# Kernel optimization log

Measured on AMD Instinct MI355X. Metric: run time of the kernel, lower is better.

Reference implementation:

```python
import jax, jax.numpy as jnp
import numpy as np
from jax import lax

B, H, W, C = 4, 32, 32, 256
N_HEADS = 8
HEAD_D = C // N_HEADS  # 32


def position_encoding(height, width, channels):
    # Faithful to Position_Embedding: for size=256, dim=128; both even/odd use sin.
    dim = channels // 2
    y_embed = np.repeat(np.arange(1, height + 1), width).reshape(height, width)
    x_embed = np.broadcast_to(np.arange(1, width + 1), (height, width))
    div_term = 10000.0 ** (2 * (np.arange(dim) // 2) / dim)
    pos_x = x_embed[:, :, None] / div_term
    pos_y = y_embed[:, :, None] / div_term
    px = np.concatenate((np.sin(pos_x[:, :, 0::2]), np.sin(pos_x[:, :, 1::2])), axis=2)
    py = np.concatenate((np.sin(pos_y[:, :, 0::2]), np.sin(pos_y[:, :, 1::2])), axis=2)
    pe = np.concatenate((py, px), axis=2)[None].astype(np.float32)  # [1,H,W,C]
    return jnp.asarray(pe)


def setup_inputs() -> dict:
    key = jax.random.key(0)
    ks = jax.random.split(key, 10)
    s = 0.02  # weight init scale
    return {
        "src1": jax.random.normal(ks[0], (B, H, W, C), jnp.float32),
        "src2": jax.random.normal(ks[1], (B, H, W, C), jnp.float32),
        "Wq1": jax.random.normal(ks[2], (C, C), jnp.float32) * s,
        "bq1": jnp.zeros((C,), jnp.float32),
        "Wq2": jax.random.normal(ks[3], (C, C), jnp.float32) * s,
        "bq2": jnp.zeros((C,), jnp.float32),
        "Wk": jax.random.normal(ks[4], (C, C), jnp.float32) * s,
        "bk": jnp.zeros((C,), jnp.float32),
        "Wv": jax.random.normal(ks[5], (C, C), jnp.float32) * s,
        "bv": jnp.zeros((C,), jnp.float32),
        "conv_w": jax.random.normal(ks[6], (3, 3, 2 * HEAD_D, 2 * HEAD_D), jnp.float32) * s,
        "conv_b": jnp.zeros((2 * HEAD_D,), jnp.float32),
        "Wo": jax.random.normal(ks[7], (C, C), jnp.float32) * s,
        "bo": jnp.zeros((C,), jnp.float32),
    }


def reference(src1, src2, Wq1, bq1, Wq2, bq2, Wk, bk, Wv, bv, conv_w, conv_b, Wo, bo):
    d = HEAD_D
    N = H * W
    pe = position_encoding(H, W, C)  # [1,H,W,C]
    kin = src1 + pe
    q1_in = src1 + pe
    v_in = src1 + pe
    q2_in = src2 + pe

    q1 = q1_in @ Wq1 + bq1  # [B,H,W,C]
    q2 = q2_in @ Wq2 + bq2
    k = kin @ Wk + bk
    v = v_in @ Wv + bv

    # Q head split: 8 heads -> add first 4 and last 4 -> 4 effective heads
    Q1 = q1.reshape(B, N, 8, d)
    q_s_1 = Q1[:, :, :4, :] + Q1[:, :, 4:, :]  # [B,N,4,d]
    Q2 = q2.reshape(B, N, 8, d)
    q_s_2 = Q2[:, :, :4, :] + Q2[:, :, 4:, :]  # [B,N,4,d]

    # K split: self path (first 4d channels), co path (conv on 2d, concat last 2d)
    k_s = k[..., : 4 * d]  # [B,H,W,4d]
    k_co_1 = k[..., 4 * d : 6 * d]  # [B,H,W,2d]
    k_co_2 = k[..., 6 * d :]  # [B,H,W,2d]
    k_conv_r = lax.conv_general_dilated(
        k_co_1, conv_w, window_strides=(1, 1), padding="SAME",
        dimension_numbers=("NHWC", "HWIO", "NHWC")) + conv_b
    k_conv = jnp.concatenate([k_conv_r, k_co_2], axis=-1)  # [B,H,W,4d]

    k_s_1 = k_s.reshape(B, N, 4, d)
    k_s_2 = k_conv.reshape(B, N, 4, d)
    v_co = v.reshape(B, N, 8, d).transpose(0, 2, 1, 3)  # [B,8,N,d]

    scale = jnp.sqrt(jnp.float32(d))
    logits_self = jnp.einsum("bnhd,bmhd->bhnm", q_s_1, k_s_1) / scale  # [B,4,N,N]
    logits_co = jnp.einsum("bnhd,bmhd->bhnm", q_s_2, k_s_2) / scale  # [B,4,N,N]
    scaled = jnp.concatenate([logits_co, logits_self], axis=1)  # [B,8,N,N]

    attn = jax.nn.softmax(scaled, axis=-1)
    out = jnp.einsum("bhnm,bhmd->bnhd", attn, v_co).reshape(B, N, C)
    return out @ Wo + bo  # [B,N,C]
```

## Files before the change

kernel.cpp:

```cpp
#include <hip/hip_runtime.h>
#include <cstdint>
#include <cstddef>

typedef __attribute__((ext_vector_type(8))) short short8v;
typedef __attribute__((ext_vector_type(4))) short short4v;
typedef __attribute__((ext_vector_type(4))) float f32x4;
typedef unsigned short ushort_t;

__device__ inline unsigned short f2bf(float x) {
    unsigned int u = __float_as_uint(x);
    return (unsigned short)((u + 0x7FFFu + ((u >> 16) & 1u)) >> 16);
}

__device__ inline unsigned int cvtpk_bf16(float lo, float hi) {
    unsigned int r;
    asm("v_cvt_pk_bf16_f32 %0, %1, %2" : "=v"(r) : "v"(lo), "v"(hi));
    return r;
}

__global__ __launch_bounds__(256) void pe_prep_kernel(
    const float* __restrict__ src1, const float* __restrict__ src2,
    const float* __restrict__ Wq1, const float* __restrict__ Wq2,
    const float* __restrict__ Wk, const float* __restrict__ Wv,
    const float* __restrict__ Wo, const float* __restrict__ cw,
    const float* __restrict__ bq1, const float* __restrict__ bq2,
    const float* __restrict__ bk, const float* __restrict__ bv,
    ushort_t* __restrict__ X1, ushort_t* __restrict__ X2,
    ushort_t* __restrict__ WcatT, ushort_t* __restrict__ WoT,
    float* __restrict__ bcat, ushort_t* __restrict__ Wcv2)
{
    __shared__ ushort_t Ts[64][72];
    int bx = blockIdx.x;
    int t = threadIdx.x;

    if (bx < 512) {
        int n = bx * 2 + (t >> 7);
        int cp = (t & 127) * 2;
        int row = n >> 5, col = n & 31;
        float pos = (cp < 128) ? (float)(row + 1) : (float)(col + 1);
        float f0 = expf(-0.14391156831212787f * (float)(cp & 63));
        float f1 = expf(-0.14391156831212787f * (float)((cp + 1) & 63));
        float pe0 = sinf(pos * f0);
        float pe1 = sinf(pos * f1);
        #pragma unroll
        for (int b = 0; b < 4; ++b) {
            size_t idx = ((size_t)b * 1024 + n) * 256 + cp;
            float2 s1 = *(const float2*)&src1[idx];
            float2 s2 = *(const float2*)&src2[idx];
            *(unsigned int*)&X1[idx] = cvtpk_bf16(s1.x + pe0, s1.y + pe1);
            *(unsigned int*)&X2[idx] = cvtpk_bf16(s2.x + pe0, s2.y + pe1);
        }
        return;
    }

    if (bx < 576) {
        int idx = bx - 512;
        int kt = idx & 3, ct = idx >> 2;
        int k0 = kt * 64;
        const float* W; int csrc; int fold = 0; ushort_t* dst; int dstbase;
        if (ct < 2)       { W = Wq1; csrc = ct * 64;        fold = 1; dst = WcatT; dstbase = ct * 64; }
        else if (ct < 4)  { W = Wq2; csrc = (ct - 2) * 64;  fold = 1; dst = WcatT; dstbase = ct * 64; }
        else if (ct < 8)  { W = Wk;  csrc = (ct - 4) * 64;            dst = WcatT; dstbase = ct * 64; }
        else if (ct < 12) { W = Wv;  csrc = (ct - 8) * 64;            dst = WcatT; dstbase = ct * 64; }
        else              { W = Wo;  csrc = (ct - 12) * 64;           dst = WoT;   dstbase = (ct - 12) * 64; }
        if (kt == 0) {
            if (ct == 0 && t < 128) bcat[t] = bq1[t] + bq1[t + 128];
            if (ct == 2 && t < 128) bcat[128 + t] = bq2[t] + bq2[t + 128];
            if (ct == 4) bcat[256 + t] = bk[t];
            if (ct == 8) bcat[512 + t] = bv[t];
        }

        int kr = t >> 2, cq = t & 3;
        #pragma unroll
        for (int i = 0; i < 4; ++i) {
            int cc = cq * 16 + i * 4;
            float4 v = *(const float4*)&W[(size_t)(k0 + kr) * 256 + csrc + cc];
            if (fold) {
                float4 v2 = *(const float4*)&W[(size_t)(k0 + kr) * 256 + csrc + cc + 128];
                v.x += v2.x; v.y += v2.y; v.z += v2.z; v.w += v2.w;
            }
            unsigned int u01 = cvtpk_bf16(v.x, v.y);
            unsigned int u23 = cvtpk_bf16(v.z, v.w);
            Ts[kr][cc + 0] = (ushort_t)(u01 & 0xFFFFu); Ts[kr][cc + 1] = (ushort_t)(u01 >> 16);
            Ts[kr][cc + 2] = (ushort_t)(u23 & 0xFFFFu); Ts[kr][cc + 3] = (ushort_t)(u23 >> 16);
        }
        __syncthreads();
        int cr = t >> 2, kq = t & 3;
        ushort_t tmp[16];
        #pragma unroll
        for (int i = 0; i < 16; ++i) tmp[i] = Ts[kq * 16 + i][cr];
        *(short8v*)&dst[(size_t)(dstbase + cr) * 256 + k0 + kq * 16]     = *(short8v*)&tmp[0];
        *(short8v*)&dst[(size_t)(dstbase + cr) * 256 + k0 + kq * 16 + 8] = *(short8v*)&tmp[8];
        return;
    }

    {
        int tap = bx - 576;
        int ci = t >> 2, co0 = (t & 3) * 16;
        #pragma unroll
        for (int i = 0; i < 16; ++i)
            Ts[ci][co0 + i] = f2bf(cw[((size_t)(tap * 64 + ci)) * 64 + co0 + i]);
        __syncthreads();
        int co = t >> 2, ci0 = (t & 3) * 16;
        ushort_t tmp[16];
        #pragma unroll
        for (int i = 0; i < 16; ++i) tmp[i] = Ts[ci0 + i][co];
        int kh = ci0 >> 5;
        int f = (tap * 2 + kh) * 4 + (co >> 4);
        int off = f * 512 + (co & 15) * 32 + (ci0 & 31);
        *(short8v*)&Wcv2[off]     = *(short8v*)&tmp[0];
        *(short8v*)&Wcv2[off + 8] = *(short8v*)&tmp[8];
    }
}

__global__ __launch_bounds__(256) void proj_gemm(
    const ushort_t* __restrict__ X1, const ushort_t* __restrict__ X2,
    const ushort_t* __restrict__ WcatT, const float* __restrict__ bcat,
    ushort_t* __restrict__ Qbf, ushort_t* __restrict__ Kbf,
    ushort_t* __restrict__ VTbf, ushort_t* __restrict__ CVbf)
{
    __shared__ ushort_t As[64][136];
    __shared__ ushort_t Bs[64][136];
    int colBase = blockIdx.x * 64, rowBase = blockIdx.y * 64;
    const ushort_t* A = (colBase >= 128 && colBase < 256) ? X2 : X1;
    int tid = threadIdx.x;
    int w = tid >> 6, l = tid & 63, lr = l & 15, g = l >> 4;
    int wr = w >> 1, wc = w & 1;
    int tr = tid >> 2, tq = tid & 3;
    f32x4 acc[2][2] = {};

    for (int kb = 0; kb < 256; kb += 128) {
        #pragma unroll
        for (int i = 0; i < 4; ++i)
            *(short8v*)&As[tr][tq * 32 + i * 8] =
                *(const short8v*)&A[(size_t)(rowBase + tr) * 256 + kb + tq * 32 + i * 8];
        #pragma unroll
        for (int i = 0; i < 4; ++i)
            *(short8v*)&Bs[tr][tq * 32 + i * 8] =
                *(const short8v*)&WcatT[(size_t)(colBase + tr) * 256 + kb + tq * 32 + i * 8];
        __syncthreads();
        #pragma unroll
        for (int ks = 0; ks < 4; ++ks) {
            short8v a0 = *(const short8v*)&As[wr * 32 + lr][ks * 32 + g * 8];
            short8v a1 = *(const short8v*)&As[wr * 32 + 16 + lr][ks * 32 + g * 8];
            short8v b0 = *(const short8v*)&Bs[wc * 32 + lr][ks * 32 + g * 8];
            short8v b1 = *(const short8v*)&Bs[wc * 32 + 16 + lr][ks * 32 + g * 8];
            acc[0][0] = __builtin_amdgcn_mfma_f32_16x16x32_bf16(a0, b0, acc[0][0], 0, 0, 0);
            acc[0][1] = __builtin_amdgcn_mfma_f32_16x16x32_bf16(a0, b1, acc[0][1], 0, 0, 0);
            acc[1][0] = __builtin_amdgcn_mfma_f32_16x16x32_bf16(a1, b0, acc[1][0], 0, 0, 0);
            acc[1][1] = __builtin_amdgcn_mfma_f32_16x16x32_bf16(a1, b1, acc[1][1], 0, 0, 0);
        }
        __syncthreads();
    }

    const float scale = 0.25503532182457352f;
    #pragma unroll
    for (int fr = 0; fr < 2; ++fr)
        #pragma unroll
        for (int fc = 0; fc < 2; ++fc) {
            int c = colBase + wc * 32 + fc * 16 + lr;
            float bv = bcat[c];
            int nb = rowBase + wr * 32 + fr * 16 + g * 4;
            int b = nb >> 10;
            float vv[4];
            #pragma unroll
            for (int r = 0; r < 4; ++r) vv[r] = acc[fr][fc][r] + bv;
            if (c < 256) {
                #pragma unroll
                for (int r = 0; r < 4; ++r) vv[r] *= scale;
            }
            unsigned int u01 = cvtpk_bf16(vv[0], vv[1]);
            unsigned int u23 = cvtpk_bf16(vv[2], vv[3]);
            ushort_t sv[4] = {(ushort_t)(u01 & 0xFFFFu), (ushort_t)(u01 >> 16),
                              (ushort_t)(u23 & 0xFFFFu), (ushort_t)(u23 >> 16)};
            if (c < 512) {
                #pragma unroll
                for (int r = 0; r < 4; ++r) {
                    int n = nb + r;
                    if (c < 128) {
                        int h = 4 + (c >> 5), d = c & 31;
                        Qbf[(((size_t)(b * 8 + h) << 10) | (n & 1023)) * 32 + d] = sv[r];
                    } else if (c < 256) {
                        int c2 = c - 128;
                        int h = c2 >> 5, d = c2 & 31;
                        Qbf[(((size_t)(b * 8 + h) << 10) | (n & 1023)) * 32 + d] = sv[r];
                    } else {
                        int c3 = c - 256;
                        if (c3 < 128) {
                            int h = 4 + (c3 >> 5), d = c3 & 31;
                            Kbf[(((size_t)(b * 8 + h) << 10) | (n & 1023)) * 32 + d] = sv[r];
                        } else if (c3 < 192) {
                            CVbf[(size_t)n * 64 + (c3 - 128)] = sv[r];
                        } else {
                            int h = 2 + ((c3 - 192) >> 5), d = c3 & 31;
                            Kbf[(((size_t)(b * 8 + h) << 10) | (n & 1023)) * 32 + d] = sv[r];
                        }
                    }
                }
            } else {
                int c4 = c - 512;
                int h = c4 >> 5, d = c4 & 31;
                uint2 pk;
                pk.x = u01; pk.y = u23;
                *(uint2*)&VTbf[((size_t)((b * 8 + h) * 32 + d)) * 1024 + (nb & 1023)] = pk;
            }
        }
}

__global__ __launch_bounds__(256) void conv_mfma(
    const ushort_t* __restrict__ CVbf, const ushort_t* __restrict__ Wcv2,
    const float* __restrict__ cb, ushort_t* __restrict__ Kbf)
{
    __shared__ ushort_t Xs[8704];
    int blk = blockIdx.x;
    int b = blk >> 5, rem = blk & 31;
    int y0 = (rem >> 1) * 2, chalf = rem & 1;
    int tid = threadIdx.x, w = tid >> 6, l = tid & 63, lr = l & 15, g = l >> 4;

    for (int p = tid >> 1; p < 136; p += 128) {
        int ry = p / 34, xc = p % 34;
        int ci0 = (tid & 1) * 32;
        int gy = y0 - 1 + ry, gx = xc - 1;
        int base = p << 6;
        int sw = (xc & 7) << 3;
        if ((unsigned)gy < 32u && (unsigned)gx < 32u) {
            const ushort_t* src = &CVbf[((size_t)(b * 1024 + gy * 32 + gx)) * 64 + ci0];
            #pragma unroll
            for (int k = 0; k < 4; ++k)
                *(short8v*)&Xs[(base + ci0 + k * 8) ^ sw] = *(const short8v*)&src[k * 8];
        } else {
            short8v z = {};
            #pragma unroll
            for (int k = 0; k < 4; ++k)
                *(short8v*)&Xs[(base + ci0 + k * 8) ^ sw] = z;
        }
    }
    __syncthreads();

    int yl = w >> 1, xb = (w & 1) * 16;
    f32x4 acc[2] = {};
    #pragma unroll
    for (int ky = 0; ky < 3; ++ky)
        #pragma unroll
        for (int kx = 0; kx < 3; ++kx) {
            int tap = ky * 3 + kx;
            #pragma unroll
            for (int kh = 0; kh < 2; ++kh) {
                int xa = xb + lr + kx;
                int e = (((yl + ky) * 34 + xa) << 6) + kh * 32 + g * 8;
                short8v af = *(const short8v*)&Xs[e ^ ((xa & 7) << 3)];
                int fb = ((tap * 2 + kh) * 4 + chalf * 2) * 512 + lr * 32 + g * 8;
                #pragma unroll
                for (int nf = 0; nf < 2; ++nf) {
                    short8v bf_ = *(const short8v*)&Wcv2[fb + nf * 512];
                    acc[nf] = __builtin_amdgcn_mfma_f32_16x16x32_bf16(af, bf_, acc[nf], 0, 0, 0);
                }
            }
        }

    #pragma unroll
    for (int nf = 0; nf < 2; ++nf) {
        int co = chalf * 32 + nf * 16 + lr;
        float bias = cb[co];
        int h = chalf, d = nf * 16 + lr;
        unsigned int u01 = cvtpk_bf16(acc[nf][0] + bias, acc[nf][1] + bias);
        unsigned int u23 = cvtpk_bf16(acc[nf][2] + bias, acc[nf][3] + bias);
        ushort_t sv[4] = {(ushort_t)(u01 & 0xFFFFu), (ushort_t)(u01 >> 16),
                          (ushort_t)(u23 & 0xFFFFu), (ushort_t)(u23 >> 16)};
        #pragma unroll
        for (int r = 0; r < 4; ++r) {
            int px = w * 16 + g * 4 + r;
            int n = y0 * 32 + px;
            Kbf[(((size_t)(b * 8 + h) << 10) | n) * 32 + d] = sv[r];
        }
    }
}

__global__ __launch_bounds__(256) void attn_mfma6(
    const ushort_t* __restrict__ Qbf, const ushort_t* __restrict__ Kbf,
    const ushort_t* __restrict__ VTbf, ushort_t* __restrict__ AObf)
{
    __shared__ ushort_t Kt[2][128][32];
    __shared__ ushort_t VT[2][32][136];
    __shared__ ushort_t Ps[4][16][136];

    int bh = blockIdx.y, q0 = blockIdx.x * 64;
    int tid = threadIdx.x, w = tid >> 6, l = tid & 63, lr = l & 15, g = l >> 4;
    int vd = tid >> 3, vn = (tid & 7) * 8;

    short8v qfrag = *(const short8v*)&Qbf[((size_t)bh * 1024 + q0 + w * 16 + lr) * 32 + g * 8];

    f32x4 accO[2] = {};
    float lsum = 0.f;
    const f32x4 zero = {};

    const short8v* Ksrc = (const short8v*)&Kbf[(size_t)bh * 1024 * 32];
    const ushort_t* Vsrc = &VTbf[(size_t)bh * 32 * 1024];

    ((short8v*)&Kt[0][0][0])[tid]       = Ksrc[tid];
    ((short8v*)&Kt[0][0][0])[tid + 256] = Ksrc[tid + 256];
    *(short8v*)&VT[0][vd][vn]      = *(const short8v*)&Vsrc[(size_t)vd * 1024 + vn];
    *(short8v*)&VT[0][vd][vn + 64] = *(const short8v*)&Vsrc[(size_t)vd * 1024 + vn + 64];

    for (int mt = 0; mt < 8; ++mt) {
        int cur = mt & 1, nb = cur ^ 1;
        __syncthreads();

        short8v kreg0, kreg1, vreg0, vreg1;
        bool hasNext = (mt + 1) < 8;
        if (hasNext) {
            int m1 = (mt + 1) * 128;
            kreg0 = Ksrc[m1 * 4 + tid];
            kreg1 = Ksrc[m1 * 4 + tid + 256];
            vreg0 = *(const short8v*)&Vsrc[(size_t)vd * 1024 + m1 + vn];
            vreg1 = *(const short8v*)&Vsrc[(size_t)vd * 1024 + m1 + vn + 64];
        }

        f32x4 st[8];
        #pragma unroll
        for (int t = 0; t < 8; ++t) {
            short8v kf = *(const short8v*)&Kt[cur][t * 16 + lr][g * 8];
            st[t] = __builtin_amdgcn_mfma_f32_16x16x32_bf16(kf, qfrag, zero, 0, 0, 0);
        }

        #pragma unroll
        for (int t = 0; t < 8; ++t) {
            float p0 = exp2f(st[t][0]), p1 = exp2f(st[t][1]);
            float p2 = exp2f(st[t][2]), p3 = exp2f(st[t][3]);
            lsum += (p0 + p1) + (p2 + p3);
            uint2 pw;
            pw.x = cvtpk_bf16(p0, p1);
            pw.y = cvtpk_bf16(p2, p3);
            *(uint2*)&Ps[w][lr][t * 16 + g * 4] = pw;
        }

        #pragma unroll
        for (int kt = 0; kt < 4; ++kt) {
            short8v pa = *(const short8v*)&Ps[w][lr][kt * 32 + g * 8];
            #pragma unroll
            for (int nt = 0; nt < 2; ++nt) {
                short8v vb = *(const short8v*)&VT[cur][nt * 16 + lr][kt * 32 + g * 8];
                accO[nt] = __builtin_amdgcn_mfma_f32_16x16x32_bf16(pa, vb, accO[nt], 0, 0, 0);
            }
        }

        if (hasNext) {
            ((short8v*)&Kt[nb][0][0])[tid]       = kreg0;
            ((short8v*)&Kt[nb][0][0])[tid + 256] = kreg1;
            *(short8v*)&VT[nb][vd][vn]      = vreg0;
            *(short8v*)&VT[nb][vd][vn + 64] = vreg1;
        }
    }

    lsum += __shfl_xor(lsum, 16);
    lsum += __shfl_xor(lsum, 32);

    int b = bh >> 3, h = bh & 7;
    #pragma unroll
    for (int r = 0; r < 4; ++r) {
        float lv = __uint_as_float((unsigned)__builtin_amdgcn_ds_bpermute(
            (g * 4 + r) * 4, (int)__float_as_uint(lsum)));
        float inv = 1.0f / lv;
        int n = q0 + w * 16 + g * 4 + r;
        unsigned int u = cvtpk_bf16(accO[0][r] * inv, accO[1][r] * inv);
        AObf[((size_t)(b * 1024 + n)) * 256 + h * 32 + lr]      = (ushort_t)(u & 0xFFFFu);
        AObf[((size_t)(b * 1024 + n)) * 256 + h * 32 + 16 + lr] = (ushort_t)(u >> 16);
    }
}

__global__ __launch_bounds__(256) void out_gemm(
    const ushort_t* __restrict__ A, const ushort_t* __restrict__ WoT,
    const float* __restrict__ bo, float* __restrict__ out)
{
    __shared__ ushort_t As[64][136];
    __shared__ ushort_t Bs[64][136];
    int colBase = blockIdx.x * 64, rowBase = blockIdx.y * 64;
    int tid = threadIdx.x;
    int w = tid >> 6, l = tid & 63, lr = l & 15, g = l >> 4;
    int wr = w >> 1, wc = w & 1;
    int tr = tid >> 2, tq = tid & 3;
    f32x4 acc[2][2] = {};

    for (int kb = 0; kb < 256; kb += 128) {
        #pragma unroll
        for (int i = 0; i < 4; ++i)
            *(short8v*)&As[tr][tq * 32 + i * 8] =
                *(const short8v*)&A[(size_t)(rowBase + tr) * 256 + kb + tq * 32 + i * 8];
        #pragma unroll
        for (int i = 0; i < 4; ++i)
            *(short8v*)&Bs[tr][tq * 32 + i * 8] =
                *(const short8v*)&WoT[(size_t)(colBase + tr) * 256 + kb + tq * 32 + i * 8];
        __syncthreads();
        #pragma unroll
        for (int ks = 0; ks < 4; ++ks) {
            short8v a0 = *(const short8v*)&As[wr * 32 + lr][ks * 32 + g * 8];
            short8v a1 = *(const short8v*)&As[wr * 32 + 16 + lr][ks * 32 + g * 8];
            short8v b0 = *(const short8v*)&Bs[wc * 32 + lr][ks * 32 + g * 8];
            short8v b1 = *(const short8v*)&Bs[wc * 32 + 16 + lr][ks * 32 + g * 8];
            acc[0][0] = __builtin_amdgcn_mfma_f32_16x16x32_bf16(a0, b0, acc[0][0], 0, 0, 0);
            acc[0][1] = __builtin_amdgcn_mfma_f32_16x16x32_bf16(a0, b1, acc[0][1], 0, 0, 0);
            acc[1][0] = __builtin_amdgcn_mfma_f32_16x16x32_bf16(a1, b0, acc[1][0], 0, 0, 0);
            acc[1][1] = __builtin_amdgcn_mfma_f32_16x16x32_bf16(a1, b1, acc[1][1], 0, 0, 0);
        }
        __syncthreads();
    }

    #pragma unroll
    for (int fr = 0; fr < 2; ++fr)
        #pragma unroll
        for (int fc = 0; fc < 2; ++fc) {
            int c = colBase + wc * 32 + fc * 16 + lr;
            float bv = bo[c];
            int nb = rowBase + wr * 32 + fr * 16 + g * 4;
            #pragma unroll
            for (int r = 0; r < 4; ++r)
                out[(size_t)(nb + r) * 256 + c] = acc[fr][fc][r] + bv;
        }
}

extern "C" void kernel_launch(void* const* d_in, const int* in_sizes, int n_in,
                              void* d_out, int out_size, void* d_ws, size_t ws_size,
                              hipStream_t stream)
{
    const float* src1 = (const float*)d_in[0];
    const float* src2 = (const float*)d_in[1];
    const float* Wq1  = (const float*)d_in[2];
    const float* bq1  = (const float*)d_in[3];
    const float* Wq2  = (const float*)d_in[4];
    const float* bq2  = (const float*)d_in[5];
    const float* Wk   = (const float*)d_in[6];
    const float* bk   = (const float*)d_in[7];
    const float* Wv   = (const float*)d_in[8];
    const float* bv   = (const float*)d_in[9];
    const float* cw   = (const float*)d_in[10];
    const float* cb   = (const float*)d_in[11];
    const float* Wo   = (const float*)d_in[12];
    const float* bo   = (const float*)d_in[13];
    float* out = (float*)d_out;

    char* base = (char*)d_ws;
    const size_t MB = 1u << 20;
    const size_t KB = 1u << 10;
    ushort_t* X1bf = (ushort_t*)(base + 0 * MB);
    ushort_t* X2bf = (ushort_t*)(base + 2 * MB);
    ushort_t* Qbf  = (ushort_t*)(base + 4 * MB);
    ushort_t* Kbf  = (ushort_t*)(base + 6 * MB);
    ushort_t* VTbf = (ushort_t*)(base + 8 * MB);
    ushort_t* AObf = (ushort_t*)(base + 10 * MB);
    ushort_t* CVbf = (ushort_t*)(base + 12 * MB);
    ushort_t* WcatT= (ushort_t*)(base + 12 * MB + 512 * KB);
    ushort_t* WoT  = (ushort_t*)(base + 12 * MB + 896 * KB);
    float*    bcat = (float*)(base + 13 * MB);
    ushort_t* Wcv2 = (ushort_t*)(base + 13 * MB + 4 * KB);

    pe_prep_kernel<<<585, 256, 0, stream>>>(
        src1, src2, Wq1, Wq2, Wk, Wv, Wo, cw, bq1, bq2, bk, bv,
        X1bf, X2bf, WcatT, WoT, bcat, Wcv2);
    proj_gemm<<<dim3(12, 64), 256, 0, stream>>>(
        X1bf, X2bf, WcatT, bcat, Qbf, Kbf, VTbf, CVbf);
    conv_mfma<<<128, 256, 0, stream>>>(CVbf, Wcv2, cb, Kbf);
    attn_mfma6<<<dim3(16, 32), 256, 0, stream>>>(Qbf, Kbf, VTbf, AObf);
    out_gemm<<<dim3(4, 64), 256, 0, stream>>>(AObf, WoT, bo, out);
}
```

Measured before the change: 45.94 us.

## Compute conv-input K slice in prep kernel and merge projection with conv launch

```diff
diff --git a/kernel.cpp b/kernel.cpp
--- a/kernel.cpp
+++ b/kernel.cpp
@@ -27,14 +27,17 @@
     const float* __restrict__ bk, const float* __restrict__ bv,
     ushort_t* __restrict__ X1, ushort_t* __restrict__ X2,
     ushort_t* __restrict__ WcatT, ushort_t* __restrict__ WoT,
-    float* __restrict__ bcat, ushort_t* __restrict__ Wcv2)
+    float* __restrict__ bcat, ushort_t* __restrict__ Wcv2,
+    ushort_t* __restrict__ CVbf)
 {
     __shared__ ushort_t Ts[64][72];
+    __shared__ float XF[8][256];
     int bx = blockIdx.x;
     int t = threadIdx.x;
 
     if (bx < 512) {
-        int n = bx * 2 + (t >> 7);
+        int nl = t >> 7;
+        int n = bx * 2 + nl;
         int cp = (t & 127) * 2;
         int row = n >> 5, col = n & 31;
         float pos = (cp < 128) ? (float)(row + 1) : (float)(col + 1);
@@ -47,9 +50,36 @@
             size_t idx = ((size_t)b * 1024 + n) * 256 + cp;
             float2 s1 = *(const float2*)&src1[idx];
             float2 s2 = *(const float2*)&src2[idx];
-            *(unsigned int*)&X1[idx] = cvtpk_bf16(s1.x + pe0, s1.y + pe1);
+            float x0 = s1.x + pe0, x1 = s1.y + pe1;
+            *(unsigned int*)&X1[idx] = cvtpk_bf16(x0, x1);
             *(unsigned int*)&X2[idx] = cvtpk_bf16(s2.x + pe0, s2.y + pe1);
-        }
+            XF[b * 2 + nl][cp]     = x0;
+            XF[b * 2 + nl][cp + 1] = x1;
+        }
+        __syncthreads();
+
+        int j = t & 63, grp = t >> 6;
+        const float* wkp = Wk + 128 + j;
+        float biasj = bk[128 + j];
+        float a0 = 0.f, a1 = 0.f, b0 = 0.f, b1 = 0.f;
+        float c0 = 0.f, c1 = 0.f, d0 = 0.f, d1 = 0.f;
+        #pragma unroll 4
+        for (int c = 0; c < 256; c += 4) {
+            float w0 = wkp[(size_t)(c + 0) * 256];
+            float w1 = wkp[(size_t)(c + 1) * 256];
+            float w2 = wkp[(size_t)(c + 2) * 256];
+            float w3 = wkp[(size_t)(c + 3) * 256];
+            a0 += XF[grp][c]     * w0;  a1 += XF[grp + 4][c]     * w0;
+            b0 += XF[grp][c + 1] * w1;  b1 += XF[grp + 4][c + 1] * w1;
+            c0 += XF[grp][c + 2] * w2;  c1 += XF[grp + 4][c + 2] * w2;
+            d0 += XF[grp][c + 3] * w3;  d1 += XF[grp + 4][c + 3] * w3;
+        }
+        float r0 = (a0 + b0) + (c0 + d0) + biasj;
+        float r1 = (a1 + b1) + (c1 + d1) + biasj;
+        int rb0 = grp >> 1,       rn0 = bx * 2 + (grp & 1);
+        int rb1 = (grp + 4) >> 1, rn1 = bx * 2 + ((grp + 4) & 1);
+        CVbf[((size_t)(rb0 * 1024 + rn0)) * 64 + j] = f2bf(r0);
+        CVbf[((size_t)(rb1 * 1024 + rn1)) * 64 + j] = f2bf(r1);
         return;
     }
 
@@ -113,165 +143,167 @@
     }
 }
 
-__global__ __launch_bounds__(256) void proj_gemm(
+__global__ __launch_bounds__(256) void proj_conv(
     const ushort_t* __restrict__ X1, const ushort_t* __restrict__ X2,
     const ushort_t* __restrict__ WcatT, const float* __restrict__ bcat,
     ushort_t* __restrict__ Qbf, ushort_t* __restrict__ Kbf,
-    ushort_t* __restrict__ VTbf, ushort_t* __restrict__ CVbf)
+    ushort_t* __restrict__ VTbf,
+    const ushort_t* __restrict__ CVbf, const ushort_t* __restrict__ Wcv2,
+    const float* __restrict__ cb)
 {
-    __shared__ ushort_t As[64][136];
-    __shared__ ushort_t Bs[64][136];
-    int colBase = blockIdx.x * 64, rowBase = blockIdx.y * 64;
-    const ushort_t* A = (colBase >= 128 && colBase < 256) ? X2 : X1;
+    __shared__ ushort_t SMEM[17408];
+    int bx = blockIdx.x;
     int tid = threadIdx.x;
     int w = tid >> 6, l = tid & 63, lr = l & 15, g = l >> 4;
-    int wr = w >> 1, wc = w & 1;
-    int tr = tid >> 2, tq = tid & 3;
-    f32x4 acc[2][2] = {};
-
-    for (int kb = 0; kb < 256; kb += 128) {
-        #pragma unroll
-        for (int i = 0; i < 4; ++i)
-            *(short8v*)&As[tr][tq * 32 + i * 8] =
-                *(const short8v*)&A[(size_t)(rowBase + tr) * 256 + kb + tq * 32 + i * 8];
-        #pragma unroll
-        for (int i = 0; i < 4; ++i)
-            *(short8v*)&Bs[tr][tq * 32 + i * 8] =
-                *(const short8v*)&WcatT[(size_t)(colBase + tr) * 256 + kb + tq * 32 + i * 8];
-        __syncthreads();
-        #pragma unroll
-        for (int ks = 0; ks < 4; ++ks) {
-            short8v a0 = *(const short8v*)&As[wr * 32 + lr][ks * 32 + g * 8];
-            short8v a1 = *(const short8v*)&As[wr * 32 + 16 + lr][ks * 32 + g * 8];
-            short8v b0 = *(const short8v*)&Bs[wc * 32 + lr][ks * 32 + g * 8];
-            short8v b1 = *(const short8v*)&Bs[wc * 32 + 16 + lr][ks * 32 + g * 8];
-            acc[0][0] = __builtin_amdgcn_mfma_f32_16x16x32_bf16(a0, b0, acc[0][0], 0, 0, 0);
-            acc[0][1] = __builtin_amdgcn_mfma_f32_16x16x32_bf16(a0, b1, acc[0][1], 0, 0, 0);
-            acc[1][0] = __builtin_amdgcn_mfma_f32_16x16x32_bf16(a1, b0, acc[1][0], 0, 0, 0);
-            acc[1][1] = __builtin_amdgcn_mfma_f32_16x16x32_bf16(a1, b1, acc[1][1], 0, 0, 0);
-        }
-        __syncthreads();
-    }
-
-    const float scale = 0.25503532182457352f;
-    #pragma unroll
-    for (int fr = 0; fr < 2; ++fr)
-        #pragma unroll
-        for (int fc = 0; fc < 2; ++fc) {
-            int c = colBase + wc * 32 + fc * 16 + lr;
-            float bv = bcat[c];
-            int nb = rowBase + wr * 32 + fr * 16 + g * 4;
-            int b = nb >> 10;
-            float vv[4];
-            #pragma unroll
-            for (int r = 0; r < 4; ++r) vv[r] = acc[fr][fc][r] + bv;
-            if (c < 256) {
+
+    if (bx < 768) {
+        ushort_t (*As)[136] = (ushort_t(*)[136])SMEM;
+        ushort_t (*Bs)[136] = (ushort_t(*)[136])(SMEM + 8704);
+        int colBase = (bx % 12) * 64, rowBase = (bx / 12) * 64;
+        const ushort_t* A = (colBase >= 128 && colBase < 256) ? X2 : X1;
+        int wr = w >> 1, wc = w & 1;
+        int tr = tid >> 2, tq = tid & 3;
+        f32x4 acc[2][2] = {};
+
+        for (int kb = 0; kb < 256; kb += 128) {
+            #pragma unroll
+            for (int i = 0; i < 4; ++i)
+                *(short8v*)&As[tr][tq * 32 + i * 8] =
+                    *(const short8v*)&A[(size_t)(rowBase + tr) * 256 + kb + tq * 32 + i * 8];
+            #pragma unroll
+            for (int i = 0; i < 4; ++i)
+                *(short8v*)&Bs[tr][tq * 32 + i * 8] =
+                    *(const short8v*)&WcatT[(size_t)(colBase + tr) * 256 + kb + tq * 32 + i * 8];
+            __syncthreads();
+            #pragma unroll
+            for (int ks = 0; ks < 4; ++ks) {
+                short8v a0 = *(const short8v*)&As[wr * 32 + lr][ks * 32 + g * 8];
+                short8v a1 = *(const short8v*)&As[wr * 32 + 16 + lr][ks * 32 + g * 8];
+                short8v b0 = *(const short8v*)&Bs[wc * 32 + lr][ks * 32 + g * 8];
+                short8v b1 = *(const short8v*)&Bs[wc * 32 + 16 + lr][ks * 32 + g * 8];
+                acc[0][0] = __builtin_amdgcn_mfma_f32_16x16x32_bf16(a0, b0, acc[0][0], 0, 0, 0);
+                acc[0][1] = __builtin_amdgcn_mfma_f32_16x16x32_bf16(a0, b1, acc[0][1], 0, 0, 0);
+                acc[1][0] = __builtin_amdgcn_mfma_f32_16x16x32_bf16(a1, b0, acc[1][0], 0, 0, 0);
+                acc[1][1] = __builtin_amdgcn_mfma_f32_16x16x32_bf16(a1, b1, acc[1][1], 0, 0, 0);
+            }
+            __syncthreads();
+        }
+
+        const float scale = 0.25503532182457352f;
+        #pragma unroll
+        for (int fr = 0; fr < 2; ++fr)
+            #pragma unroll
+            for (int fc = 0; fc < 2; ++fc) {
+                int c = colBase + wc * 32 + fc * 16 + lr;
+                float bv = bcat[c];
+                int nb = rowBase + wr * 32 + fr * 16 + g * 4;
+                int b = nb >> 10;
+                float vv[4];
                 #pragma unroll
-                for (int r = 0; r < 4; ++r) vv[r] *= scale;
-            }
-            unsigned int u01 = cvtpk_bf16(vv[0], vv[1]);
-            unsigned int u23 = cvtpk_bf16(vv[2], vv[3]);
+                for (int r = 0; r < 4; ++r) vv[r] = acc[fr][fc][r] + bv;
+                if (c < 256) {
+                    #pragma unroll
+                    for (int r = 0; r < 4; ++r) vv[r] *= scale;
+                }
+                unsigned int u01 = cvtpk_bf16(vv[0], vv[1]);
+                unsigned int u23 = cvtpk_bf16(vv[2], vv[3]);
+                ushort_t sv[4] = {(ushort_t)(u01 & 0xFFFFu), (ushort_t)(u01 >> 16),
+                                  (ushort_t)(u23 & 0xFFFFu), (ushort_t)(u23 >> 16)};
+                if (c < 512) {
+                    #pragma unroll
+                    for (int r = 0; r < 4; ++r) {
+                        int n = nb + r;
+                        if (c < 128) {
+                            int h = 4 + (c >> 5), d = c & 31;
+                            Qbf[(((size_t)(b * 8 + h) << 10) | (n & 1023)) * 32 + d] = sv[r];
+                        } else if (c < 256) {
+                            int c2 = c - 128;
+                            int h = c2 >> 5, d = c2 & 31;
+                            Qbf[(((size_t)(b * 8 + h) << 10) | (n & 1023)) * 32 + d] = sv[r];
+                        } else {
+                            int c3 = c - 256;
+                            if (c3 < 128) {
+                                int h = 4 + (c3 >> 5), d = c3 & 31;
+                                Kbf[(((size_t)(b * 8 + h) << 10) | (n & 1023)) * 32 + d] = sv[r];
+                            } else if (c3 >= 192) {
+                                int h = 2 + ((c3 - 192) >> 5), d = c3 & 31;
+                                Kbf[(((size_t)(b * 8 + h) << 10) | (n & 1023)) * 32 + d] = sv[r];
+                            }
+                        }
+                    }
+                } else {
+                    int c4 = c - 512;
+                    int h = c4 >> 5, d = c4 & 31;
+                    uint2 pk;
+                    pk.x = u01; pk.y = u23;
+                    *(uint2*)&VTbf[((size_t)((b * 8 + h) * 32 + d)) * 1024 + (nb & 1023)] = pk;
+                }
+            }
+        return;
+    }
+
+    {
+        ushort_t* Xs = SMEM;
+        int blk = bx - 768;
+        int b = blk >> 5, rem = blk & 31;
+        int y0 = (rem >> 1) * 2, chalf = rem & 1;
+
+        for (int p = tid >> 1; p < 136; p += 128) {
+            int ry = p / 34, xc = p % 34;
+            int ci0 = (tid & 1) * 32;
+            int gy = y0 - 1 + ry, gx = xc - 1;
+            int base = p << 6;
+            int sw = (xc & 7) << 3;
+            if ((unsigned)gy < 32u && (unsigned)gx < 32u) {
+                const ushort_t* src = &CVbf[((size_t)(b * 1024 + gy * 32 + gx)) * 64 + ci0];
+                #pragma unroll
+                for (int k = 0; k < 4; ++k)
+                    *(short8v*)&Xs[(base + ci0 + k * 8) ^ sw] = *(const short8v*)&src[k * 8];
+            } else {
+                short8v z = {};
+                #pragma unroll
+                for (int k = 0; k < 4; ++k)
+                    *(short8v*)&Xs[(base + ci0 + k * 8) ^ sw] = z;
+            }
+        }
+        __syncthreads();
+
+        int yl = w >> 1, xb = (w & 1) * 16;
+        f32x4 acc[2] = {};
+        #pragma unroll
+        for (int ky = 0; ky < 3; ++ky)
+            #pragma unroll
+            for (int kx = 0; kx < 3; ++kx) {
+                int tap = ky * 3 + kx;
+                #pragma unroll
+                for (int kh = 0; kh < 2; ++kh) {
+                    int xa = xb + lr + kx;
+                    int e = (((yl + ky) * 34 + xa) << 6) + kh * 32 + g * 8;
+                    short8v af = *(const short8v*)&Xs[e ^ ((xa & 7) << 3)];
+                    int fb = ((tap * 2 + kh) * 4 + chalf * 2) * 512 + lr * 32 + g * 8;
+                    #pragma unroll
+                    for (int nf = 0; nf < 2; ++nf) {
+                        short8v bf_ = *(const short8v*)&Wcv2[fb + nf * 512];
+                        acc[nf] = __builtin_amdgcn_mfma_f32_16x16x32_bf16(af, bf_, acc[nf], 0, 0, 0);
+                    }
+                }
+            }
+
+        #pragma unroll
+        for (int nf = 0; nf < 2; ++nf) {
+            int co = chalf * 32 + nf * 16 + lr;
+            float bias = cb[co];
+            int h = chalf, d = nf * 16 + lr;
+            unsigned int u01 = cvtpk_bf16(acc[nf][0] + bias, acc[nf][1] + bias);
+            unsigned int u23 = cvtpk_bf16(acc[nf][2] + bias, acc[nf][3] + bias);
             ushort_t sv[4] = {(ushort_t)(u01 & 0xFFFFu), (ushort_t)(u01 >> 16),
                               (ushort_t)(u23 & 0xFFFFu), (ushort_t)(u23 >> 16)};
-            if (c < 512) {
-                #pragma unroll
-                for (int r = 0; r < 4; ++r) {
-                    int n = nb + r;
-                    if (c < 128) {
-                        int h = 4 + (c >> 5), d = c & 31;
-                        Qbf[(((size_t)(b * 8 + h) << 10) | (n & 1023)) * 32 + d] = sv[r];
-                    } else if (c < 256) {
-                        int c2 = c - 128;
-                        int h = c2 >> 5, d = c2 & 31;
-                        Qbf[(((size_t)(b * 8 + h) << 10) | (n & 1023)) * 32 + d] = sv[r];
-                    } else {
-                        int c3 = c - 256;
-                        if (c3 < 128) {
-                            int h = 4 + (c3 >> 5), d = c3 & 31;
-                            Kbf[(((size_t)(b * 8 + h) << 10) | (n & 1023)) * 32 + d] = sv[r];
-                        } else if (c3 < 192) {
-                            CVbf[(size_t)n * 64 + (c3 - 128)] = sv[r];
-                        } else {
-                            int h = 2 + ((c3 - 192) >> 5), d = c3 & 31;
-                            Kbf[(((size_t)(b * 8 + h) << 10) | (n & 1023)) * 32 + d] = sv[r];
-                        }
-                    }
-                }
-            } else {
-                int c4 = c - 512;
-                int h = c4 >> 5, d = c4 & 31;
-                uint2 pk;
-                pk.x = u01; pk.y = u23;
-                *(uint2*)&VTbf[((size_t)((b * 8 + h) * 32 + d)) * 1024 + (nb & 1023)] = pk;
-            }
-        }
-}
-
-__global__ __launch_bounds__(256) void conv_mfma(
-    const ushort_t* __restrict__ CVbf, const ushort_t* __restrict__ Wcv2,
-    const float* __restrict__ cb, ushort_t* __restrict__ Kbf)
-{
-    __shared__ ushort_t Xs[8704];
-    int blk = blockIdx.x;
-    int b = blk >> 5, rem = blk & 31;
-    int y0 = (rem >> 1) * 2, chalf = rem & 1;
-    int tid = threadIdx.x, w = tid >> 6, l = tid & 63, lr = l & 15, g = l >> 4;
-
-    for (int p = tid >> 1; p < 136; p += 128) {
-        int ry = p / 34, xc = p % 34;
-        int ci0 = (tid & 1) * 32;
-        int gy = y0 - 1 + ry, gx = xc - 1;
-        int base = p << 6;
-        int sw = (xc & 7) << 3;
-        if ((unsigned)gy < 32u && (unsigned)gx < 32u) {
-            const ushort_t* src = &CVbf[((size_t)(b * 1024 + gy * 32 + gx)) * 64 + ci0];
-            #pragma unroll
-            for (int k = 0; k < 4; ++k)
-                *(short8v*)&Xs[(base + ci0 + k * 8) ^ sw] = *(const short8v*)&src[k * 8];
-        } else {
-            short8v z = {};
-            #pragma unroll
-            for (int k = 0; k < 4; ++k)
-                *(short8v*)&Xs[(base + ci0 + k * 8) ^ sw] = z;
-        }
-    }
-    __syncthreads();
-
-    int yl = w >> 1, xb = (w & 1) * 16;
-    f32x4 acc[2] = {};
-    #pragma unroll
-    for (int ky = 0; ky < 3; ++ky)
-        #pragma unroll
-        for (int kx = 0; kx < 3; ++kx) {
-            int tap = ky * 3 + kx;
-            #pragma unroll
-            for (int kh = 0; kh < 2; ++kh) {
-                int xa = xb + lr + kx;
-                int e = (((yl + ky) * 34 + xa) << 6) + kh * 32 + g * 8;
-                short8v af = *(const short8v*)&Xs[e ^ ((xa & 7) << 3)];
-                int fb = ((tap * 2 + kh) * 4 + chalf * 2) * 512 + lr * 32 + g * 8;
-                #pragma unroll
-                for (int nf = 0; nf < 2; ++nf) {
-                    short8v bf_ = *(const short8v*)&Wcv2[fb + nf * 512];
-                    acc[nf] = __builtin_amdgcn_mfma_f32_16x16x32_bf16(af, bf_, acc[nf], 0, 0, 0);
-                }
-            }
-        }
-
-    #pragma unroll
-    for (int nf = 0; nf < 2; ++nf) {
-        int co = chalf * 32 + nf * 16 + lr;
-        float bias = cb[co];
-        int h = chalf, d = nf * 16 + lr;
-        unsigned int u01 = cvtpk_bf16(acc[nf][0] + bias, acc[nf][1] + bias);
-        unsigned int u23 = cvtpk_bf16(acc[nf][2] + bias, acc[nf][3] + bias);
-        ushort_t sv[4] = {(ushort_t)(u01 & 0xFFFFu), (ushort_t)(u01 >> 16),
-                          (ushort_t)(u23 & 0xFFFFu), (ushort_t)(u23 >> 16)};
-        #pragma unroll
-        for (int r = 0; r < 4; ++r) {
-            int px = w * 16 + g * 4 + r;
-            int n = y0 * 32 + px;
-            Kbf[(((size_t)(b * 8 + h) << 10) | n) * 32 + d] = sv[r];
+            #pragma unroll
+            for (int r = 0; r < 4; ++r) {
+                int px = w * 16 + g * 4 + r;
+                int n = y0 * 32 + px;
+                Kbf[(((size_t)(b * 8 + h) << 10) | n) * 32 + d] = sv[r];
+            }
         }
     }
 }
@@ -455,10 +487,9 @@
 
     pe_prep_kernel<<<585, 256, 0, stream>>>(
         src1, src2, Wq1, Wq2, Wk, Wv, Wo, cw, bq1, bq2, bk, bv,
-        X1bf, X2bf, WcatT, WoT, bcat, Wcv2);
-    proj_gemm<<<dim3(12, 64), 256, 0, stream>>>(
-        X1bf, X2bf, WcatT, bcat, Qbf, Kbf, VTbf, CVbf);
-    conv_mfma<<<128, 256, 0, stream>>>(CVbf, Wcv2, cb, Kbf);
+        X1bf, X2bf, WcatT, WoT, bcat, Wcv2, CVbf);
+    proj_conv<<<896, 256, 0, stream>>>(
+        X1bf, X2bf, WcatT, bcat, Qbf, Kbf, VTbf, CVbf, Wcv2, cb);
     attn_mfma6<<<dim3(16, 32), 256, 0, stream>>>(Qbf, Kbf, VTbf, AObf);
     out_gemm<<<dim3(4, 64), 256, 0, stream>>>(AObf, WoT, bo, out);
 }
```

Measured after the change: 46.45 us. About the same (+1.1%).
